# Optimization experiments

Hardware: AMD Instinct MI355X
Metric: run time of the kernel (lower is better)

Reference implementation:

```python
import jax, jax.numpy as jnp
import numpy as np

NEG_SLOPE = 0.2  # PyG GATConv default negative_slope


def gat_conv(x, src, dst, W, a_src, a_dst, b, n_nodes, concat):
    # x: [N, F_in]; W: [F_in, H*C]; a_src/a_dst: [H, C]; b: [H*C] or [C]
    H, C = a_src.shape
    h = (x @ W).reshape(n_nodes, H, C)                      # [N, H, C]
    al_src = jnp.sum(h * a_src[None], axis=-1)              # [N, H]
    al_dst = jnp.sum(h * a_dst[None], axis=-1)              # [N, H]
    e = jax.nn.leaky_relu(al_src[src] + al_dst[dst], NEG_SLOPE)  # [E, H]
    # segment softmax over incoming edges of each destination node
    m = jax.ops.segment_max(e, dst, num_segments=n_nodes)  # [N, H]
    ex = jnp.exp(e - m[dst])                                # [E, H]
    s = jax.ops.segment_sum(ex, dst, num_segments=n_nodes)  # [N, H]
    alpha = ex / s[dst]                                     # [E, H]
    msg = h[src] * alpha[:, :, None]                        # [E, H, C]
    out = jax.ops.segment_sum(msg, dst, num_segments=n_nodes)  # [N, H, C]
    if concat:
        out = out.reshape(n_nodes, H * C)
    else:
        out = out.mean(axis=1)
    return out + b


def setup_inputs() -> dict:
    key = jax.random.key(0)
    ks = jax.random.split(key, 10)
    N, E = 100000, 800000
    F_in, C1, H, C2 = 128, 32, 8, 16
    x = jax.random.normal(ks[0], (N, F_in), dtype=jnp.float32)
    edge_index = jax.random.randint(ks[1], (2, E), 0, N, dtype=jnp.int64)
    s = 0.05
    return {
        "x": x,
        "edge_index": edge_index,
        "W1": jax.random.normal(ks[2], (F_in, H * C1), dtype=jnp.float32) * s,
        "att_src1": jax.random.normal(ks[3], (H, C1), dtype=jnp.float32) * s,
        "att_dst1": jax.random.normal(ks[4], (H, C1), dtype=jnp.float32) * s,
        "b1": jnp.zeros((H * C1,), dtype=jnp.float32),
        "W2": jax.random.normal(ks[5], (H * C1, H * C2), dtype=jnp.float32) * s,
        "att_src2": jax.random.normal(ks[6], (H, C2), dtype=jnp.float32) * s,
        "att_dst2": jax.random.normal(ks[7], (H, C2), dtype=jnp.float32) * s,
        "b2": jnp.zeros((C2,), dtype=jnp.float32),
    }


def reference(x, edge_index, W1, att_src1, att_dst1, b1, W2, att_src2, att_dst2, b2):
    n = x.shape[0]
    # PyG GATConv default add_self_loops=True (same augmented edge set for both layers)
    loops = jnp.arange(n, dtype=edge_index.dtype)
    src = jnp.concatenate([edge_index[0], loops])
    dst = jnp.concatenate([edge_index[1], loops])
    # dropout_p = 0.0 -> dropout is identity (eval-mode math)
    h = gat_conv(x, src, dst, W1, att_src1, att_dst1, b1, n, concat=True)
    h = jax.nn.elu(h)
    out = gat_conv(h, src, dst, W2, att_src2, att_dst2, b2, n, concat=False)
    return jax.nn.log_softmax(out, axis=-1)
```

## Files before the change

kernel.cpp:

```cpp
#include <hip/hip_runtime.h>
#include <cstdint>
#include <cstddef>


typedef short bf16x8 __attribute__((ext_vector_type(8)));
typedef unsigned short u16x8 __attribute__((ext_vector_type(8)));
typedef float f32x4 __attribute__((ext_vector_type(4)));

__device__ inline unsigned short f2bf(float f) {
  unsigned u = __float_as_uint(f);
  unsigned r = (u + 0x7FFFu + ((u >> 16) & 1u)) >> 16;
  return (unsigned short)r;
}
__device__ inline float bf2f(unsigned short s) {
  return __uint_as_float((unsigned)s << 16);
}


__global__ __launch_bounds__(256) void detect_kernel(const int* __restrict__ words,
                                                     int E, int* __restrict__ flag) {
  int t = threadIdx.x;
  int n = E < 1024 ? E : 1024;
  int cnt = 0;
  for (int i = t; i < n; i += 256) cnt += (words[2 * i + 1] != 0) ? 1 : 0;
  for (int m = 1; m < 64; m <<= 1) cnt += __shfl_xor(cnt, m);
  if ((t & 63) == 0 && cnt) atomicAdd(flag, cnt);
}

__global__ __launch_bounds__(256) void extract_kernel(const void* __restrict__ ei,
                                                      int E, int N,
                                                      const int* __restrict__ flag,
                                                      int* __restrict__ src,
                                                      int* __restrict__ dst,
                                                      int* __restrict__ deg) {
  int e = blockIdx.x * 256 + threadIdx.x;
  int ET = E + N;
  if (e >= ET) return;
  int s, d;
  if (e < E) {
    if (flag[0] == 0) {
      const long long* p = (const long long*)ei;
      s = (int)p[e];
      d = (int)p[(size_t)E + e];
    } else {
      const int* p = (const int*)ei;
      s = p[e];
      d = p[E + e];
    }
  } else {
    s = d = e - E;
  }
  src[e] = s;
  dst[e] = d;
  atomicAdd(&deg[d], 1);
}

__global__ __launch_bounds__(256) void scan_a(const int* __restrict__ deg,
                                              int* __restrict__ off,
                                              int* __restrict__ bsum, int N) {
  __shared__ int sh[256];
  int b = blockIdx.x, t = threadIdx.x;
  int base = b * 2048 + t * 8;
  int p[8];
  int run = 0;
#pragma unroll
  for (int j = 0; j < 8; ++j) {
    int v = (base + j < N) ? deg[base + j] : 0;
    run += v;
    p[j] = run;
  }
  sh[t] = run;
  __syncthreads();
  for (int d = 1; d < 256; d <<= 1) {
    int x = (t >= d) ? sh[t - d] : 0;
    __syncthreads();
    if (t >= d) sh[t] += x;
    __syncthreads();
  }
  int excl = sh[t] - run;
#pragma unroll
  for (int j = 0; j < 8; ++j)
    if (base + j < N) off[base + j + 1] = excl + p[j];
  if (t == 255) bsum[b] = sh[255];
}

__global__ void scan_b(int* __restrict__ bsum, int nb) {
  int run = 0;
  for (int i = 0; i < nb; ++i) {
    int v = bsum[i];
    bsum[i] = run;
    run += v;
  }
}

__global__ __launch_bounds__(256) void scan_c(int* __restrict__ off,
                                              const int* __restrict__ bsum, int N) {
  int i = blockIdx.x * 256 + threadIdx.x;
  if (i == 0) off[0] = 0;
  if (i >= 1 && i <= N) off[i] += bsum[(i - 1) / 2048];
}

__global__ __launch_bounds__(256) void fill_kernel(const int* __restrict__ src,
                                                   const int* __restrict__ dst,
                                                   const int* __restrict__ off,
                                                   int* __restrict__ deg,
                                                   int* __restrict__ csr, int ET) {
  int e = blockIdx.x * 256 + threadIdx.x;
  if (e >= ET) return;
  int d = dst[e];
  int p = atomicSub(&deg[d], 1) - 1;
  csr[off[d] + p] = src[e];
}

__global__ __launch_bounds__(256) void pack_kernel(const float* __restrict__ W,
                                                   short* __restrict__ Wp,
                                                   int NOUT, int total) {
  int NT = NOUT >> 4;
  for (int idx = blockIdx.x * 256 + threadIdx.x; idx < total;
       idx += gridDim.x * 256) {
    int j = idx & 7;
    int lane = (idx >> 3) & 63;
    int st = idx >> 9;
    int s = st / NT, t = st - s * NT;
    int k = s * 32 + (lane >> 4) * 8 + j;
    int n = t * 16 + (lane & 15);
    Wp[idx] = (short)f2bf(W[(size_t)k * NOUT + n]);
  }
}

template <int K, int NOUT, bool AF32>
__global__ __launch_bounds__(256) void mfma_gemm(const void* __restrict__ Av,
                                                 const short* __restrict__ Bp,
                                                 short* __restrict__ Cb,
                                                 const float* __restrict__ as,
                                                 const float* __restrict__ ad,
                                                 float* __restrict__ alsO,
                                                 float* __restrict__ aldO, int M) {
  constexpr int KS = K / 32;
  constexpr int NT = NOUT / 16;
  constexpr int RST = NOUT + 8;
  constexpr int C = NOUT / 8;
  __shared__ __align__(16) short lds[64 * RST];
  const int tid = threadIdx.x;
  const int wave = tid >> 6, lane = tid & 63;
  const int lo = lane & 15, hi = lane >> 4;
  const int rowA = blockIdx.x * 64 + wave * 16 + lo;
  const bool inb = rowA < M;

  f32x4 acc[NT];
#pragma unroll
  for (int t = 0; t < NT; ++t) acc[t] = (f32x4){0.f, 0.f, 0.f, 0.f};

#pragma unroll
  for (int s = 0; s < KS; ++s) {
    bf16x8 af;
    if constexpr (AF32) {
      const float* Ap = (const float*)Av;
      float v[8];
      if (inb) {
        const float4 x0 = *(const float4*)&Ap[(size_t)rowA * K + s * 32 + hi * 8];
        const float4 x1 = *(const float4*)&Ap[(size_t)rowA * K + s * 32 + hi * 8 + 4];
        v[0] = x0.x; v[1] = x0.y; v[2] = x0.z; v[3] = x0.w;
        v[4] = x1.x; v[5] = x1.y; v[6] = x1.z; v[7] = x1.w;
      } else {
#pragma unroll
        for (int j = 0; j < 8; ++j) v[j] = 0.f;
      }
#pragma unroll
      for (int j = 0; j < 8; ++j) af[j] = (short)f2bf(v[j]);
    } else {
      const short* Ab = (const short*)Av;
      if (inb) {
        af = *(const bf16x8*)&Ab[(size_t)rowA * K + s * 32 + hi * 8];
      } else {
#pragma unroll
        for (int j = 0; j < 8; ++j) af[j] = 0;
      }
    }
#pragma unroll
    for (int t = 0; t < NT; ++t) {
      bf16x8 bf = *(const bf16x8*)&Bp[((size_t)(s * NT + t) * 64 + lane) * 8];
      acc[t] = __builtin_amdgcn_mfma_f32_16x16x32_bf16(af, bf, acc[t], 0, 0, 0);
    }
  }

#pragma unroll
  for (int t = 0; t < NT; ++t)
#pragma unroll
    for (int r = 0; r < 4; ++r)
      lds[(wave * 16 + hi * 4 + r) * RST + t * 16 + lo] = (short)f2bf(acc[t][r]);
  __syncthreads();

  constexpr int VECS = 64 * NOUT / 8;
#pragma unroll
  for (int i = 0; i < VECS / 256; ++i) {
    int v = i * 256 + tid;
    int r = v / (NOUT / 8);
    int c = v % (NOUT / 8);
    int grow = blockIdx.x * 64 + r;
    if (grow < M)
      *(float4*)&Cb[(size_t)grow * NOUT + c * 8] =
          *(const float4*)&lds[r * RST + c * 8];
  }

  constexpr int SEGS = NOUT / 64;
  if (tid < 64 * SEGS) {
    int r = tid / SEGS, seg = tid % SEGS;
    int grow = blockIdx.x * 64 + r;
    float ps[8], pd[8];
#pragma unroll
    for (int k = 0; k < 8; ++k) { ps[k] = 0.f; pd[k] = 0.f; }
#pragma unroll
    for (int k = 0; k < 8; ++k) {
      int b = seg + SEGS * k;
      u16x8 u = *(const u16x8*)&lds[r * RST + b * 8];
#pragma unroll
      for (int j = 0; j < 8; ++j) {
        float hv = bf2f(u[j]);
        ps[k] = fmaf(hv, as[k * C + seg * 8 + j], ps[k]);
        pd[k] = fmaf(hv, ad[k * C + seg * 8 + j], pd[k]);
      }
    }
#pragma unroll
    for (int d = 1; d < SEGS; d <<= 1)
#pragma unroll
      for (int k = 0; k < 8; ++k) {
        ps[k] += __shfl_xor(ps[k], d);
        pd[k] += __shfl_xor(pd[k], d);
      }
    if (seg == 0 && grow < M) {
      *(float4*)&alsO[(size_t)grow * 8] = make_float4(ps[0], ps[1], ps[2], ps[3]);
      *(float4*)&alsO[(size_t)grow * 8 + 4] = make_float4(ps[4], ps[5], ps[6], ps[7]);
      *(float4*)&aldO[(size_t)grow * 8] = make_float4(pd[0], pd[1], pd[2], pd[3]);
      *(float4*)&aldO[(size_t)grow * 8 + 4] = make_float4(pd[4], pd[5], pd[6], pd[7]);
    }
  }
}

template <int LAYER>
__global__ __launch_bounds__(256) void agg_kernel(const short* __restrict__ hb,
                                                  const float* __restrict__ als,
                                                  const float* __restrict__ ald,
                                                  const int* __restrict__ off,
                                                  const int* __restrict__ csr,
                                                  const float* __restrict__ bias,
                                                  void* __restrict__ outv, int N) {
  constexpr int C = (LAYER == 1) ? 32 : 16;
  constexpr int ROW = 8 * C;
  constexpr int LPG = ROW / 8;
  constexpr int NS = 64 / LPG;
  int wid = blockIdx.x * 4 + (threadIdx.x >> 6);
  if (wid >= N) return;
  int lane = threadIdx.x & 63;
  int rs = off[wid], re = off[wid + 1];
  int stream = lane / LPG;
  int gl = lane & (LPG - 1);
  int head = (gl * 8) / C;
  float aldv = ald[(size_t)wid * 8 + head];

  float acc[8];
#pragma unroll
  for (int j = 0; j < 8; ++j) acc[j] = 0.f;
  float ws = 0.f;

  int i = rs + stream;
  for (; i + NS < re; i += 2 * NS) {
    int s0 = csr[i], s1 = csr[i + NS];
    float e0 = als[(size_t)s0 * 8 + head] + aldv;
    float e1 = als[(size_t)s1 * 8 + head] + aldv;
    u16x8 u0 = *(const u16x8*)&hb[(size_t)s0 * ROW + gl * 8];
    u16x8 u1 = *(const u16x8*)&hb[(size_t)s1 * ROW + gl * 8];
    e0 = e0 > 0.f ? e0 : 0.2f * e0;
    e1 = e1 > 0.f ? e1 : 0.2f * e1;
    float w0 = __expf(e0), w1 = __expf(e1);
    ws += w0 + w1;
#pragma unroll
    for (int j = 0; j < 8; ++j)
      acc[j] = fmaf(w1, bf2f(u1[j]), fmaf(w0, bf2f(u0[j]), acc[j]));
  }
  if (i < re) {
    int s0 = csr[i];
    float e0 = als[(size_t)s0 * 8 + head] + aldv;
    u16x8 u0 = *(const u16x8*)&hb[(size_t)s0 * ROW + gl * 8];
    e0 = e0 > 0.f ? e0 : 0.2f * e0;
    float w0 = __expf(e0);
    ws += w0;
#pragma unroll
    for (int j = 0; j < 8; ++j) acc[j] = fmaf(w0, bf2f(u0[j]), acc[j]);
  }

#pragma unroll
  for (int d = LPG; d < 64; d <<= 1) {
    ws += __shfl_xor(ws, d);
#pragma unroll
    for (int j = 0; j < 8; ++j) acc[j] += __shfl_xor(acc[j], d);
  }
  float inv = 1.f / ws;

  if constexpr (LAYER == 1) {
    if (lane < 32) {
      u16x8 o;
#pragma unroll
      for (int j = 0; j < 8; ++j) {
        float v = acc[j] * inv + bias[gl * 8 + j];
        o[j] = f2bf(v > 0.f ? v : expm1f(v));
      }
      *(u16x8*)&((short*)outv)[(size_t)wid * 256 + gl * 8] = o;
    }
  } else {
#pragma unroll
    for (int j = 0; j < 8; ++j) acc[j] *= inv;
#pragma unroll
    for (int d = 2; d <= 8; d <<= 1)
#pragma unroll
      for (int j = 0; j < 8; ++j) acc[j] += __shfl_xor(acc[j], d);
    int p = gl & 1;
    float v[8];
#pragma unroll
    for (int j = 0; j < 8; ++j) v[j] = acc[j] * 0.125f + bias[p * 8 + j];
    float m = v[0];
#pragma unroll
    for (int j = 1; j < 8; ++j) m = fmaxf(m, v[j]);
    m = fmaxf(m, __shfl_xor(m, 1));
    float se = 0.f;
#pragma unroll
    for (int j = 0; j < 8; ++j) se += __expf(v[j] - m);
    se += __shfl_xor(se, 1);
    float lse = m + logf(se);
    if (lane < 2) {
      float* out = (float*)outv;
      *(float4*)&out[(size_t)wid * 16 + p * 8] =
          make_float4(v[0] - lse, v[1] - lse, v[2] - lse, v[3] - lse);
      *(float4*)&out[(size_t)wid * 16 + p * 8 + 4] =
          make_float4(v[4] - lse, v[5] - lse, v[6] - lse, v[7] - lse);
    }
  }
}


extern "C" void kernel_launch(void* const* d_in, const int* in_sizes, int n_in,
                              void* d_out, int out_size, void* d_ws, size_t ws_size,
                              hipStream_t stream) {
  const float* x = (const float*)d_in[0];
  const void* ei = d_in[1];
  const float* W1 = (const float*)d_in[2];
  const float* as1 = (const float*)d_in[3];
  const float* ad1 = (const float*)d_in[4];
  const float* b1 = (const float*)d_in[5];
  const float* W2 = (const float*)d_in[6];
  const float* as2 = (const float*)d_in[7];
  const float* ad2 = (const float*)d_in[8];
  const float* b2 = (const float*)d_in[9];
  float* out = (float*)d_out;

  const int N = out_size / 16;
  const int E = in_sizes[1] / 2;
  const int ET = E + N;

  char* p = (char*)d_ws;
  auto alloc = [&](size_t bytes) {
    char* r = p;
    p += (bytes + 255) & ~(size_t)255;
    return (void*)r;
  };
  short* h1b = (short*)alloc((size_t)N * 256 * 2);
  short* hactb = (short*)alloc((size_t)N * 256 * 2);
  float* als = (float*)alloc((size_t)N * 8 * 4);
  float* ald = (float*)alloc((size_t)N * 8 * 4);
  int* src32 = (int*)alloc((size_t)ET * 4);
  int* dst32 = (int*)alloc((size_t)ET * 4);
  int* csr = (int*)alloc((size_t)ET * 4);
  int* deg = (int*)alloc((size_t)N * 4);
  int* off = (int*)alloc((size_t)(N + 1) * 4);
  int* bsum = (int*)alloc(256 * 4);
  int* flag = (int*)alloc(256);
  short* W1p = (short*)alloc(128 * 256 * 2);
  short* W2p = (short*)alloc(256 * 128 * 2);
  short* h2b = h1b;

  hipMemsetAsync(deg, 0, (size_t)N * 4, stream);
  hipMemsetAsync(flag, 0, 4, stream);

  detect_kernel<<<1, 256, 0, stream>>>((const int*)ei, E, flag);
  int gridET = (ET + 255) / 256;
  extract_kernel<<<gridET, 256, 0, stream>>>(ei, E, N, flag, src32, dst32, deg);
  int nscan = (N + 2047) / 2048;
  scan_a<<<nscan, 256, 0, stream>>>(deg, off, bsum, N);
  scan_b<<<1, 1, 0, stream>>>(bsum, nscan);
  scan_c<<<(N + 256) / 256, 256, 0, stream>>>(off, bsum, N);
  fill_kernel<<<gridET, 256, 0, stream>>>(src32, dst32, off, deg, csr, ET);

  pack_kernel<<<128, 256, 0, stream>>>(W1, W1p, 256, 128 * 256);
  pack_kernel<<<128, 256, 0, stream>>>(W2, W2p, 128, 256 * 128);

  int gemmGrid = (N + 63) / 64;
  int nodeGrid = (N + 3) / 4;

  mfma_gemm<128, 256, true>
      <<<gemmGrid, 256, 0, stream>>>(x, W1p, h1b, as1, ad1, als, ald, N);
  agg_kernel<1><<<nodeGrid, 256, 0, stream>>>(h1b, als, ald, off, csr, b1, hactb, N);
  mfma_gemm<256, 128, false>
      <<<gemmGrid, 256, 0, stream>>>(hactb, W2p, h2b, as2, ad2, als, ald, N);
  agg_kernel<2><<<nodeGrid, 256, 0, stream>>>(h2b, als, ald, off, csr, b2, out, N);
}
```

Before: 345.0 us.

## Split layer-1 aggregation across channel halves and software-pipeline neighbor index loads

Layer-1 aggregation now runs on a 2D grid, with each block covering 128 of the 256 channels. Every wave therefore processes 4 edge streams instead of 2, which doubles wave count and memory-level parallelism. The edge loop now prefetches the next csr indices and source attention logits one iteration ahead, using clamped indices, and folds the tail iteration into the main loop by masking the second weight. Int indexing replaces size_t. In exchange, csr and als are read twice per node for layer 1, and clamped prefetches issue redundant loads.

```diff
diff --git a/kernel.cpp b/kernel.cpp
--- a/kernel.cpp
+++ b/kernel.cpp
@@ -15,6 +15,7 @@
 __device__ inline float bf2f(unsigned short s) {
   return __uint_as_float((unsigned)s << 16);
 }
+__device__ inline int imin(int a, int b) { return a < b ? a : b; }
 
 
 __global__ __launch_bounds__(256) void detect_kernel(const int* __restrict__ words,
@@ -245,48 +246,51 @@
                                                   const int* __restrict__ csr,
                                                   const float* __restrict__ bias,
                                                   void* __restrict__ outv, int N) {
-  constexpr int C = (LAYER == 1) ? 32 : 16;
-  constexpr int ROW = 8 * C;
-  constexpr int LPG = ROW / 8;
-  constexpr int NS = 64 / LPG;
+  constexpr int ROWCH = (LAYER == 1) ? 256 : 128;
+  constexpr int HC = (LAYER == 1) ? 32 : 16;
+  constexpr int LPG = 16;
+  constexpr int NS = 4;
   int wid = blockIdx.x * 4 + (threadIdx.x >> 6);
   if (wid >= N) return;
+  int cb = blockIdx.y;
   int lane = threadIdx.x & 63;
+  int es = lane >> 4;
+  int gl = lane & (LPG - 1);
+  int chbase = cb * 128 + gl * 8;
+  int head = chbase / HC;
   int rs = off[wid], re = off[wid + 1];
-  int stream = lane / LPG;
-  int gl = lane & (LPG - 1);
-  int head = (gl * 8) / C;
-  float aldv = ald[(size_t)wid * 8 + head];
+  int relast = re - 1;
+  float aldv = ald[wid * 8 + head];
 
   float acc[8];
 #pragma unroll
   for (int j = 0; j < 8; ++j) acc[j] = 0.f;
   float ws = 0.f;
 
-  int i = rs + stream;
-  for (; i + NS < re; i += 2 * NS) {
-    int s0 = csr[i], s1 = csr[i + NS];
-    float e0 = als[(size_t)s0 * 8 + head] + aldv;
-    float e1 = als[(size_t)s1 * 8 + head] + aldv;
-    u16x8 u0 = *(const u16x8*)&hb[(size_t)s0 * ROW + gl * 8];
-    u16x8 u1 = *(const u16x8*)&hb[(size_t)s1 * ROW + gl * 8];
+  int i0 = rs + es;
+  int s0 = csr[imin(i0, relast)];
+  int s1 = csr[imin(i0 + NS, relast)];
+  float a0 = als[s0 * 8 + head];
+  float a1 = als[s1 * 8 + head];
+
+  for (int i = i0; i < re; i += 2 * NS) {
+    u16x8 u0 = *(const u16x8*)&hb[s0 * ROWCH + chbase];
+    u16x8 u1 = *(const u16x8*)&hb[s1 * ROWCH + chbase];
+    int sn0 = csr[imin(i + 2 * NS, relast)];
+    int sn1 = csr[imin(i + 3 * NS, relast)];
+    float an0 = als[sn0 * 8 + head];
+    float an1 = als[sn1 * 8 + head];
+    float e0 = a0 + aldv;
+    float e1 = a1 + aldv;
     e0 = e0 > 0.f ? e0 : 0.2f * e0;
     e1 = e1 > 0.f ? e1 : 0.2f * e1;
-    float w0 = __expf(e0), w1 = __expf(e1);
+    float w0 = __expf(e0);
+    float w1 = (i + NS < re) ? __expf(e1) : 0.f;
     ws += w0 + w1;
 #pragma unroll
     for (int j = 0; j < 8; ++j)
       acc[j] = fmaf(w1, bf2f(u1[j]), fmaf(w0, bf2f(u0[j]), acc[j]));
-  }
-  if (i < re) {
-    int s0 = csr[i];
-    float e0 = als[(size_t)s0 * 8 + head] + aldv;
-    u16x8 u0 = *(const u16x8*)&hb[(size_t)s0 * ROW + gl * 8];
-    e0 = e0 > 0.f ? e0 : 0.2f * e0;
-    float w0 = __expf(e0);
-    ws += w0;
-#pragma unroll
-    for (int j = 0; j < 8; ++j) acc[j] = fmaf(w0, bf2f(u0[j]), acc[j]);
+    s0 = sn0; s1 = sn1; a0 = an0; a1 = an1;
   }
 
 #pragma unroll
@@ -298,14 +302,14 @@
   float inv = 1.f / ws;
 
   if constexpr (LAYER == 1) {
-    if (lane < 32) {
+    if (lane < LPG) {
       u16x8 o;
 #pragma unroll
       for (int j = 0; j < 8; ++j) {
-        float v = acc[j] * inv + bias[gl * 8 + j];
+        float v = acc[j] * inv + bias[chbase + j];
         o[j] = f2bf(v > 0.f ? v : expm1f(v));
       }
-      *(u16x8*)&((short*)outv)[(size_t)wid * 256 + gl * 8] = o;
+      *(u16x8*)&((short*)outv)[wid * 256 + chbase] = o;
     }
   } else {
 #pragma unroll
@@ -398,8 +402,10 @@
 
   mfma_gemm<128, 256, true>
       <<<gemmGrid, 256, 0, stream>>>(x, W1p, h1b, as1, ad1, als, ald, N);
-  agg_kernel<1><<<nodeGrid, 256, 0, stream>>>(h1b, als, ald, off, csr, b1, hactb, N);
+  agg_kernel<1><<<dim3(nodeGrid, 2), 256, 0, stream>>>(h1b, als, ald, off, csr,
+                                                       b1, hactb, N);
   mfma_gemm<256, 128, false>
       <<<gemmGrid, 256, 0, stream>>>(hactb, W2p, h2b, as2, ad2, als, ald, N);
-  agg_kernel<2><<<nodeGrid, 256, 0, stream>>>(h2b, als, ald, off, csr, b2, out, N);
-}
+  agg_kernel<2><<<dim3(nodeGrid, 1), 256, 0, stream>>>(h2b, als, ald, off, csr,
+                                                       b2, out, N);
+}
```

After: 380.8 us. +10.4%, slower.

## Precompute per-edge attention weights in separate kernel; parallelize block-sum scan

Applied to the files above, without the earlier changes.

Adds a wpre kernel that computes exp(leaky_relu(als[src]+ald[dst])) for every edge and head once, storing the results in CSR order. The aggregation kernels then read these weights instead of recomputing them in every lane group, so they no longer gather als per edge. To support this, the fill kernel also writes the destination of each CSR slot. Separately, the serial single-thread scan_b becomes a 64-lane wavefront shuffle scan. The cost is an extra kernel launch per layer and about 29 MB of extra weight traffic written and read back per layer.

```diff
diff --git a/kernel.cpp b/kernel.cpp
--- a/kernel.cpp
+++ b/kernel.cpp
@@ -85,12 +85,14 @@
 }
 
 __global__ void scan_b(int* __restrict__ bsum, int nb) {
-  int run = 0;
-  for (int i = 0; i < nb; ++i) {
-    int v = bsum[i];
-    bsum[i] = run;
-    run += v;
-  }
+  int t = threadIdx.x;
+  int orig = (t < nb) ? bsum[t] : 0;
+  int v = orig;
+  for (int d = 1; d < 64; d <<= 1) {
+    int u = __shfl_up(v, d);
+    if (t >= d) v += u;
+  }
+  if (t < nb) bsum[t] = v - orig;
 }
 
 __global__ __launch_bounds__(256) void scan_c(int* __restrict__ off,
@@ -104,12 +106,15 @@
                                                    const int* __restrict__ dst,
                                                    const int* __restrict__ off,
                                                    int* __restrict__ deg,
-                                                   int* __restrict__ csr, int ET) {
+                                                   int* __restrict__ csr,
+                                                   int* __restrict__ dstc, int ET) {
   int e = blockIdx.x * 256 + threadIdx.x;
   if (e >= ET) return;
   int d = dst[e];
   int p = atomicSub(&deg[d], 1) - 1;
-  csr[off[d] + p] = src[e];
+  int pos = off[d] + p;
+  csr[pos] = src[e];
+  dstc[pos] = d;
 }
 
 __global__ __launch_bounds__(256) void pack_kernel(const float* __restrict__ W,
@@ -237,42 +242,51 @@
   }
 }
 
+__global__ __launch_bounds__(256) void wpre_kernel(const int* __restrict__ csr,
+                                                   const int* __restrict__ dstc,
+                                                   const float* __restrict__ als,
+                                                   const float* __restrict__ ald,
+                                                   float* __restrict__ w, int ET8) {
+  int idx = blockIdx.x * 256 + threadIdx.x;
+  if (idx >= ET8) return;
+  int pos = idx >> 3, h = idx & 7;
+  int s = csr[pos], d = dstc[pos];
+  float e = als[s * 8 + h] + ald[d * 8 + h];
+  e = e > 0.f ? e : 0.2f * e;
+  w[idx] = __expf(e);
+}
+
 template <int LAYER>
 __global__ __launch_bounds__(256) void agg_kernel(const short* __restrict__ hb,
-                                                  const float* __restrict__ als,
-                                                  const float* __restrict__ ald,
+                                                  const float* __restrict__ w,
                                                   const int* __restrict__ off,
                                                   const int* __restrict__ csr,
                                                   const float* __restrict__ bias,
                                                   void* __restrict__ outv, int N) {
-  constexpr int C = (LAYER == 1) ? 32 : 16;
-  constexpr int ROW = 8 * C;
+  constexpr int HC = (LAYER == 1) ? 32 : 16;
+  constexpr int ROW = (LAYER == 1) ? 256 : 128;
   constexpr int LPG = ROW / 8;
   constexpr int NS = 64 / LPG;
   int wid = blockIdx.x * 4 + (threadIdx.x >> 6);
   if (wid >= N) return;
   int lane = threadIdx.x & 63;
   int rs = off[wid], re = off[wid + 1];
-  int stream = lane / LPG;
+  int es = lane / LPG;
   int gl = lane & (LPG - 1);
-  int head = (gl * 8) / C;
-  float aldv = ald[(size_t)wid * 8 + head];
+  int head = (gl * 8) / HC;
 
   float acc[8];
 #pragma unroll
   for (int j = 0; j < 8; ++j) acc[j] = 0.f;
   float ws = 0.f;
 
-  int i = rs + stream;
+  int i = rs + es;
   for (; i + NS < re; i += 2 * NS) {
     int s0 = csr[i], s1 = csr[i + NS];
-    float e0 = als[(size_t)s0 * 8 + head] + aldv;
-    float e1 = als[(size_t)s1 * 8 + head] + aldv;
+    float w0 = w[i * 8 + head];
+    float w1 = w[(i + NS) * 8 + head];
     u16x8 u0 = *(const u16x8*)&hb[(size_t)s0 * ROW + gl * 8];
     u16x8 u1 = *(const u16x8*)&hb[(size_t)s1 * ROW + gl * 8];
-    e0 = e0 > 0.f ? e0 : 0.2f * e0;
-    e1 = e1 > 0.f ? e1 : 0.2f * e1;
-    float w0 = __expf(e0), w1 = __expf(e1);
     ws += w0 + w1;
 #pragma unroll
     for (int j = 0; j < 8; ++j)
@@ -280,10 +294,8 @@
   }
   if (i < re) {
     int s0 = csr[i];
-    float e0 = als[(size_t)s0 * 8 + head] + aldv;
+    float w0 = w[i * 8 + head];
     u16x8 u0 = *(const u16x8*)&hb[(size_t)s0 * ROW + gl * 8];
-    e0 = e0 > 0.f ? e0 : 0.2f * e0;
-    float w0 = __expf(e0);
     ws += w0;
 #pragma unroll
     for (int j = 0; j < 8; ++j) acc[j] = fmaf(w0, bf2f(u0[j]), acc[j]);
@@ -298,7 +310,7 @@
   float inv = 1.f / ws;
 
   if constexpr (LAYER == 1) {
-    if (lane < 32) {
+    if (lane < LPG) {
       u16x8 o;
 #pragma unroll
       for (int j = 0; j < 8; ++j) {
@@ -367,9 +379,11 @@
   short* hactb = (short*)alloc((size_t)N * 256 * 2);
   float* als = (float*)alloc((size_t)N * 8 * 4);
   float* ald = (float*)alloc((size_t)N * 8 * 4);
+  float* w = (float*)alloc((size_t)ET * 8 * 4);
   int* src32 = (int*)alloc((size_t)ET * 4);
   int* dst32 = (int*)alloc((size_t)ET * 4);
   int* csr = (int*)alloc((size_t)ET * 4);
+  int* dstc = (int*)alloc((size_t)ET * 4);
   int* deg = (int*)alloc((size_t)N * 4);
   int* off = (int*)alloc((size_t)(N + 1) * 4);
   int* bsum = (int*)alloc(256 * 4);
@@ -386,20 +400,24 @@
   extract_kernel<<<gridET, 256, 0, stream>>>(ei, E, N, flag, src32, dst32, deg);
   int nscan = (N + 2047) / 2048;
   scan_a<<<nscan, 256, 0, stream>>>(deg, off, bsum, N);
-  scan_b<<<1, 1, 0, stream>>>(bsum, nscan);
+  scan_b<<<1, 64, 0, stream>>>(bsum, nscan);
   scan_c<<<(N + 256) / 256, 256, 0, stream>>>(off, bsum, N);
-  fill_kernel<<<gridET, 256, 0, stream>>>(src32, dst32, off, deg, csr, ET);
+  fill_kernel<<<gridET, 256, 0, stream>>>(src32, dst32, off, deg, csr, dstc, ET);
 
   pack_kernel<<<128, 256, 0, stream>>>(W1, W1p, 256, 128 * 256);
   pack_kernel<<<128, 256, 0, stream>>>(W2, W2p, 128, 256 * 128);
 
   int gemmGrid = (N + 63) / 64;
   int nodeGrid = (N + 3) / 4;
+  int ET8 = ET * 8;
+  int wGrid = (ET8 + 255) / 256;
 
   mfma_gemm<128, 256, true>
       <<<gemmGrid, 256, 0, stream>>>(x, W1p, h1b, as1, ad1, als, ald, N);
-  agg_kernel<1><<<nodeGrid, 256, 0, stream>>>(h1b, als, ald, off, csr, b1, hactb, N);
+  wpre_kernel<<<wGrid, 256, 0, stream>>>(csr, dstc, als, ald, w, ET8);
+  agg_kernel<1><<<nodeGrid, 256, 0, stream>>>(h1b, w, off, csr, b1, hactb, N);
   mfma_gemm<256, 128, false>
       <<<gemmGrid, 256, 0, stream>>>(hactb, W2p, h2b, as2, ad2, als, ald, N);
-  agg_kernel<2><<<nodeGrid, 256, 0, stream>>>(h2b, als, ald, off, csr, b2, out, N);
-}
+  wpre_kernel<<<wGrid, 256, 0, stream>>>(csr, dstc, als, ald, w, ET8);
+  agg_kernel<2><<<nodeGrid, 256, 0, stream>>>(h2b, w, off, csr, b2, out, N);
+}
```

New measurement: 377.4 us. 9.4% more time.

## Store layer-1 features as FP8 for aggregation and parallelize block-sum scan

Applied to the files above, without the earlier changes.

The layer-1 GEMM now writes its projected features as FP8 E4M3 bytes, while the attention logits are still computed from the bf16 copy held in shared memory. A dedicated layer-1 aggregation kernel gathers those 8-byte FP8 chunks per lane and decodes them with the hardware FP8-to-float conversion when the builtin exists. This halves the bytes moved by the bandwidth-bound neighbour gather, at the cost of extra quantisation error in the messages. Separately, the serial single-thread block-sum scan is replaced by a 64-lane shuffle scan.

```diff
diff --git a/kernel.cpp b/kernel.cpp
--- a/kernel.cpp
+++ b/kernel.cpp
@@ -14,6 +14,42 @@
 }
 __device__ inline float bf2f(unsigned short s) {
   return __uint_as_float((unsigned)s << 16);
+}
+
+__device__ inline unsigned char fp8enc(float x) {
+  unsigned u = __float_as_uint(x);
+  unsigned s = u >> 31;
+  float ax = fminf(fabsf(x), 448.f);
+  unsigned em;
+  if (ax >= 0.015625f) {
+    unsigned b = __float_as_uint(ax);
+    unsigned b2 = b + 0x7FFFFu + ((b >> 20) & 1u);
+    em = (b2 >> 20) - 960u;
+    if (em > 126u) em = 126u;
+  } else {
+    em = (unsigned)__float2int_rn(ax * 512.f);
+  }
+  return (unsigned char)((s << 7) | em);
+}
+__device__ inline float fp8dec_sw(unsigned b8) {
+  unsigned s = b8 >> 7, em = b8 & 0x7Fu;
+  float fn = __uint_as_float((s << 31) | ((em + 960u) << 20));
+  float fd = (float)em * 0.001953125f;
+  fd = s ? -fd : fd;
+  return em >= 8u ? fn : fd;
+}
+__device__ inline void fp8dec4(unsigned w, float* out) {
+#if __has_builtin(__builtin_amdgcn_cvt_f32_fp8)
+  out[0] = __builtin_amdgcn_cvt_f32_fp8(w, 0);
+  out[1] = __builtin_amdgcn_cvt_f32_fp8(w, 1);
+  out[2] = __builtin_amdgcn_cvt_f32_fp8(w, 2);
+  out[3] = __builtin_amdgcn_cvt_f32_fp8(w, 3);
+#else
+  out[0] = fp8dec_sw(w & 0xFFu);
+  out[1] = fp8dec_sw((w >> 8) & 0xFFu);
+  out[2] = fp8dec_sw((w >> 16) & 0xFFu);
+  out[3] = fp8dec_sw((w >> 24) & 0xFFu);
+#endif
 }
 
 
@@ -85,12 +121,14 @@
 }
 
 __global__ void scan_b(int* __restrict__ bsum, int nb) {
-  int run = 0;
-  for (int i = 0; i < nb; ++i) {
-    int v = bsum[i];
-    bsum[i] = run;
-    run += v;
-  }
+  int t = threadIdx.x;
+  int orig = (t < nb) ? bsum[t] : 0;
+  int v = orig;
+  for (int d = 1; d < 64; d <<= 1) {
+    int u = __shfl_up(v, d);
+    if (t >= d) v += u;
+  }
+  if (t < nb) bsum[t] = v - orig;
 }
 
 __global__ __launch_bounds__(256) void scan_c(int* __restrict__ off,
@@ -128,10 +166,11 @@
   }
 }
 
-template <int K, int NOUT, bool AF32>
+template <int K, int NOUT, bool AF32, bool OUT_FP8>
 __global__ __launch_bounds__(256) void mfma_gemm(const void* __restrict__ Av,
                                                  const short* __restrict__ Bp,
                                                  short* __restrict__ Cb,
+                                                 unsigned char* __restrict__ Cq,
                                                  const float* __restrict__ as,
                                                  const float* __restrict__ ad,
                                                  float* __restrict__ alsO,
@@ -139,8 +178,10 @@
   constexpr int KS = K / 32;
   constexpr int NT = NOUT / 16;
   constexpr int RST = NOUT + 8;
+  constexpr int QST = NOUT + 16;
   constexpr int C = NOUT / 8;
   __shared__ __align__(16) short lds[64 * RST];
+  __shared__ __align__(16) unsigned char ldsq[OUT_FP8 ? 64 * QST : 16];
   const int tid = threadIdx.x;
   const int wave = tid >> 6, lane = tid & 63;
   const int lo = lane & 15, hi = lane >> 4;
@@ -187,20 +228,37 @@
 #pragma unroll
   for (int t = 0; t < NT; ++t)
 #pragma unroll
-    for (int r = 0; r < 4; ++r)
-      lds[(wave * 16 + hi * 4 + r) * RST + t * 16 + lo] = (short)f2bf(acc[t][r]);
+    for (int r = 0; r < 4; ++r) {
+      int row = wave * 16 + hi * 4 + r;
+      lds[row * RST + t * 16 + lo] = (short)f2bf(acc[t][r]);
+      if constexpr (OUT_FP8)
+        ldsq[row * QST + t * 16 + lo] = fp8enc(acc[t][r]);
+    }
   __syncthreads();
 
-  constexpr int VECS = 64 * NOUT / 8;
-#pragma unroll
-  for (int i = 0; i < VECS / 256; ++i) {
-    int v = i * 256 + tid;
-    int r = v / (NOUT / 8);
-    int c = v % (NOUT / 8);
-    int grow = blockIdx.x * 64 + r;
-    if (grow < M)
-      *(float4*)&Cb[(size_t)grow * NOUT + c * 8] =
-          *(const float4*)&lds[r * RST + c * 8];
+  if constexpr (OUT_FP8) {
+#pragma unroll
+    for (int i = 0; i < (64 * NOUT / 16) / 256; ++i) {
+      int v = i * 256 + tid;
+      int r = v >> 4;
+      int c = v & 15;
+      int grow = blockIdx.x * 64 + r;
+      if (grow < M)
+        *(float4*)&Cq[(size_t)grow * NOUT + c * 16] =
+            *(const float4*)&ldsq[r * QST + c * 16];
+    }
+  } else {
+    constexpr int VECS = 64 * NOUT / 8;
+#pragma unroll
+    for (int i = 0; i < VECS / 256; ++i) {
+      int v = i * 256 + tid;
+      int r = v / (NOUT / 8);
+      int c = v % (NOUT / 8);
+      int grow = blockIdx.x * 64 + r;
+      if (grow < M)
+        *(float4*)&Cb[(size_t)grow * NOUT + c * 8] =
+            *(const float4*)&lds[r * RST + c * 8];
+    }
   }
 
   constexpr int SEGS = NOUT / 64;
@@ -237,54 +295,126 @@
   }
 }
 
-template <int LAYER>
-__global__ __launch_bounds__(256) void agg_kernel(const short* __restrict__ hb,
-                                                  const float* __restrict__ als,
-                                                  const float* __restrict__ ald,
-                                                  const int* __restrict__ off,
-                                                  const int* __restrict__ csr,
-                                                  const float* __restrict__ bias,
-                                                  void* __restrict__ outv, int N) {
-  constexpr int C = (LAYER == 1) ? 32 : 16;
-  constexpr int ROW = 8 * C;
-  constexpr int LPG = ROW / 8;
-  constexpr int NS = 64 / LPG;
+__global__ __launch_bounds__(256) void agg1_kernel(const unsigned char* __restrict__ hq,
+                                                   const float* __restrict__ als,
+                                                   const float* __restrict__ ald,
+                                                   const int* __restrict__ off,
+                                                   const int* __restrict__ csr,
+                                                   const float* __restrict__ bias,
+                                                   short* __restrict__ outb, int N) {
   int wid = blockIdx.x * 4 + (threadIdx.x >> 6);
   if (wid >= N) return;
   int lane = threadIdx.x & 63;
   int rs = off[wid], re = off[wid + 1];
-  int stream = lane / LPG;
-  int gl = lane & (LPG - 1);
-  int head = (gl * 8) / C;
-  float aldv = ald[(size_t)wid * 8 + head];
+  int es = lane >> 5;
+  int gl = lane & 31;
+  int head = gl >> 2;
+  float aldv = ald[wid * 8 + head];
 
   float acc[8];
 #pragma unroll
   for (int j = 0; j < 8; ++j) acc[j] = 0.f;
   float ws = 0.f;
 
-  int i = rs + stream;
-  for (; i + NS < re; i += 2 * NS) {
-    int s0 = csr[i], s1 = csr[i + NS];
-    float e0 = als[(size_t)s0 * 8 + head] + aldv;
-    float e1 = als[(size_t)s1 * 8 + head] + aldv;
-    u16x8 u0 = *(const u16x8*)&hb[(size_t)s0 * ROW + gl * 8];
-    u16x8 u1 = *(const u16x8*)&hb[(size_t)s1 * ROW + gl * 8];
+  int i = rs + es;
+  for (; i + 2 < re; i += 4) {
+    int s0 = csr[i], s1 = csr[i + 2];
+    float e0 = als[s0 * 8 + head] + aldv;
+    float e1 = als[s1 * 8 + head] + aldv;
+    uint2 u0 = *(const uint2*)&hq[(size_t)s0 * 256 + gl * 8];
+    uint2 u1 = *(const uint2*)&hq[(size_t)s1 * 256 + gl * 8];
     e0 = e0 > 0.f ? e0 : 0.2f * e0;
     e1 = e1 > 0.f ? e1 : 0.2f * e1;
     float w0 = __expf(e0), w1 = __expf(e1);
     ws += w0 + w1;
-#pragma unroll
-    for (int j = 0; j < 8; ++j)
-      acc[j] = fmaf(w1, bf2f(u1[j]), fmaf(w0, bf2f(u0[j]), acc[j]));
+    float d0a[4], d0b[4], d1a[4], d1b[4];
+    fp8dec4(u0.x, d0a); fp8dec4(u0.y, d0b);
+    fp8dec4(u1.x, d1a); fp8dec4(u1.y, d1b);
+#pragma unroll
+    for (int j = 0; j < 4; ++j) {
+      acc[j] = fmaf(w0, d0a[j], acc[j]);
+      acc[j + 4] = fmaf(w0, d0b[j], acc[j + 4]);
+      acc[j] = fmaf(w1, d1a[j], acc[j]);
+      acc[j + 4] = fmaf(w1, d1b[j], acc[j + 4]);
+    }
   }
   if (i < re) {
     int s0 = csr[i];
-    float e0 = als[(size_t)s0 * 8 + head] + aldv;
-    u16x8 u0 = *(const u16x8*)&hb[(size_t)s0 * ROW + gl * 8];
+    float e0 = als[s0 * 8 + head] + aldv;
+    uint2 u0 = *(const uint2*)&hq[(size_t)s0 * 256 + gl * 8];
     e0 = e0 > 0.f ? e0 : 0.2f * e0;
     float w0 = __expf(e0);
     ws += w0;
+    float d0a[4], d0b[4];
+    fp8dec4(u0.x, d0a); fp8dec4(u0.y, d0b);
+#pragma unroll
+    for (int j = 0; j < 4; ++j) {
+      acc[j] = fmaf(w0, d0a[j], acc[j]);
+      acc[j + 4] = fmaf(w0, d0b[j], acc[j + 4]);
+    }
+  }
+
+  ws += __shfl_xor(ws, 32);
+#pragma unroll
+  for (int j = 0; j < 8; ++j) acc[j] += __shfl_xor(acc[j], 32);
+  float inv = 1.f / ws;
+
+  if (lane < 32) {
+    u16x8 o;
+#pragma unroll
+    for (int j = 0; j < 8; ++j) {
+      float v = acc[j] * inv + bias[gl * 8 + j];
+      o[j] = f2bf(v > 0.f ? v : expm1f(v));
+    }
+    *(u16x8*)&outb[(size_t)wid * 256 + gl * 8] = o;
+  }
+}
+
+__global__ __launch_bounds__(256) void agg2_kernel(const short* __restrict__ hb,
+                                                   const float* __restrict__ als,
+                                                   const float* __restrict__ ald,
+                                                   const int* __restrict__ off,
+                                                   const int* __restrict__ csr,
+                                                   const float* __restrict__ bias,
+                                                   float* __restrict__ out, int N) {
+  constexpr int LPG = 16;
+  constexpr int NS = 4;
+  int wid = blockIdx.x * 4 + (threadIdx.x >> 6);
+  if (wid >= N) return;
+  int lane = threadIdx.x & 63;
+  int rs = off[wid], re = off[wid + 1];
+  int es = lane / LPG;
+  int gl = lane & (LPG - 1);
+  int head = gl >> 1;
+  float aldv = ald[wid * 8 + head];
+
+  float acc[8];
+#pragma unroll
+  for (int j = 0; j < 8; ++j) acc[j] = 0.f;
+  float ws = 0.f;
+
+  int i = rs + es;
+  for (; i + NS < re; i += 2 * NS) {
+    int s0 = csr[i], s1 = csr[i + NS];
+    float e0 = als[s0 * 8 + head] + aldv;
+    float e1 = als[s1 * 8 + head] + aldv;
+    u16x8 u0 = *(const u16x8*)&hb[(size_t)s0 * 128 + gl * 8];
+    u16x8 u1 = *(const u16x8*)&hb[(size_t)s1 * 128 + gl * 8];
+    e0 = e0 > 0.f ? e0 : 0.2f * e0;
+    e1 = e1 > 0.f ? e1 : 0.2f * e1;
+    float w0 = __expf(e0), w1 = __expf(e1);
+    ws += w0 + w1;
+#pragma unroll
+    for (int j = 0; j < 8; ++j)
+      acc[j] = fmaf(w1, bf2f(u1[j]), fmaf(w0, bf2f(u0[j]), acc[j]));
+  }
+  if (i < re) {
+    int s0 = csr[i];
+    float e0 = als[s0 * 8 + head] + aldv;
+    u16x8 u0 = *(const u16x8*)&hb[(size_t)s0 * 128 + gl * 8];
+    e0 = e0 > 0.f ? e0 : 0.2f * e0;
+    float w0 = __expf(e0);
+    ws += w0;
 #pragma unroll
     for (int j = 0; j < 8; ++j) acc[j] = fmaf(w0, bf2f(u0[j]), acc[j]);
   }
@@ -297,43 +427,30 @@
   }
   float inv = 1.f / ws;
 
-  if constexpr (LAYER == 1) {
-    if (lane < 32) {
-      u16x8 o;
-#pragma unroll
-      for (int j = 0; j < 8; ++j) {
-        float v = acc[j] * inv + bias[gl * 8 + j];
-        o[j] = f2bf(v > 0.f ? v : expm1f(v));
-      }
-      *(u16x8*)&((short*)outv)[(size_t)wid * 256 + gl * 8] = o;
-    }
-  } else {
-#pragma unroll
-    for (int j = 0; j < 8; ++j) acc[j] *= inv;
-#pragma unroll
-    for (int d = 2; d <= 8; d <<= 1)
-#pragma unroll
-      for (int j = 0; j < 8; ++j) acc[j] += __shfl_xor(acc[j], d);
-    int p = gl & 1;
-    float v[8];
-#pragma unroll
-    for (int j = 0; j < 8; ++j) v[j] = acc[j] * 0.125f + bias[p * 8 + j];
-    float m = v[0];
-#pragma unroll
-    for (int j = 1; j < 8; ++j) m = fmaxf(m, v[j]);
-    m = fmaxf(m, __shfl_xor(m, 1));
-    float se = 0.f;
-#pragma unroll
-    for (int j = 0; j < 8; ++j) se += __expf(v[j] - m);
-    se += __shfl_xor(se, 1);
-    float lse = m + logf(se);
-    if (lane < 2) {
-      float* out = (float*)outv;
-      *(float4*)&out[(size_t)wid * 16 + p * 8] =
-          make_float4(v[0] - lse, v[1] - lse, v[2] - lse, v[3] - lse);
-      *(float4*)&out[(size_t)wid * 16 + p * 8 + 4] =
-          make_float4(v[4] - lse, v[5] - lse, v[6] - lse, v[7] - lse);
-    }
+#pragma unroll
+  for (int j = 0; j < 8; ++j) acc[j] *= inv;
+#pragma unroll
+  for (int d = 2; d <= 8; d <<= 1)
+#pragma unroll
+    for (int j = 0; j < 8; ++j) acc[j] += __shfl_xor(acc[j], d);
+  int p = gl & 1;
+  float v[8];
+#pragma unroll
+  for (int j = 0; j < 8; ++j) v[j] = acc[j] * 0.125f + bias[p * 8 + j];
+  float m = v[0];
+#pragma unroll
+  for (int j = 1; j < 8; ++j) m = fmaxf(m, v[j]);
+  m = fmaxf(m, __shfl_xor(m, 1));
+  float se = 0.f;
+#pragma unroll
+  for (int j = 0; j < 8; ++j) se += __expf(v[j] - m);
+  se += __shfl_xor(se, 1);
+  float lse = m + logf(se);
+  if (lane < 2) {
+    *(float4*)&out[(size_t)wid * 16 + p * 8] =
+        make_float4(v[0] - lse, v[1] - lse, v[2] - lse, v[3] - lse);
+    *(float4*)&out[(size_t)wid * 16 + p * 8 + 4] =
+        make_float4(v[4] - lse, v[5] - lse, v[6] - lse, v[7] - lse);
   }
 }
 
@@ -363,8 +480,9 @@
     p += (bytes + 255) & ~(size_t)255;
     return (void*)r;
   };
-  short* h1b = (short*)alloc((size_t)N * 256 * 2);
+  unsigned char* h1q = (unsigned char*)alloc((size_t)N * 256);
   short* hactb = (short*)alloc((size_t)N * 256 * 2);
+  short* h2b = (short*)alloc((size_t)N * 128 * 2);
   float* als = (float*)alloc((size_t)N * 8 * 4);
   float* ald = (float*)alloc((size_t)N * 8 * 4);
   int* src32 = (int*)alloc((size_t)ET * 4);
@@ -376,7 +494,6 @@
   int* flag = (int*)alloc(256);
   short* W1p = (short*)alloc(128 * 256 * 2);
   short* W2p = (short*)alloc(256 * 128 * 2);
-  short* h2b = h1b;
 
   hipMemsetAsync(deg, 0, (size_t)N * 4, stream);
   hipMemsetAsync(flag, 0, 4, stream);
@@ -386,7 +503,7 @@
   extract_kernel<<<gridET, 256, 0, stream>>>(ei, E, N, flag, src32, dst32, deg);
   int nscan = (N + 2047) / 2048;
   scan_a<<<nscan, 256, 0, stream>>>(deg, off, bsum, N);
-  scan_b<<<1, 1, 0, stream>>>(bsum, nscan);
+  scan_b<<<1, 64, 0, stream>>>(bsum, nscan);
   scan_c<<<(N + 256) / 256, 256, 0, stream>>>(off, bsum, N);
   fill_kernel<<<gridET, 256, 0, stream>>>(src32, dst32, off, deg, csr, ET);
 
@@ -396,10 +513,10 @@
   int gemmGrid = (N + 63) / 64;
   int nodeGrid = (N + 3) / 4;
 
-  mfma_gemm<128, 256, true>
-      <<<gemmGrid, 256, 0, stream>>>(x, W1p, h1b, as1, ad1, als, ald, N);
-  agg_kernel<1><<<nodeGrid, 256, 0, stream>>>(h1b, als, ald, off, csr, b1, hactb, N);
-  mfma_gemm<256, 128, false>
-      <<<gemmGrid, 256, 0, stream>>>(hactb, W2p, h2b, as2, ad2, als, ald, N);
-  agg_kernel<2><<<nodeGrid, 256, 0, stream>>>(h2b, als, ald, off, csr, b2, out, N);
-}
+  mfma_gemm<128, 256, true, true><<<gemmGrid, 256, 0, stream>>>(
+      x, W1p, nullptr, h1q, as1, ad1, als, ald, N);
+  agg1_kernel<<<nodeGrid, 256, 0, stream>>>(h1q, als, ald, off, csr, b1, hactb, N);
+  mfma_gemm<256, 128, false, false><<<gemmGrid, 256, 0, stream>>>(
+      hactb, W2p, h2b, nullptr, as2, ad2, als, ald, N);
+  agg2_kernel<<<nodeGrid, 256, 0, stream>>>(h2b, als, ald, off, csr, b2, out, N);
+}
```

After: 338.5 us. No clear change (-1.9%).
